# Optimization experiments

Measured on AMD Instinct MI355X. Metric: run time of the kernel, lower is better.

Reference implementation:

```python
import jax, jax.numpy as jnp
import numpy as np

EPS = 1e-6

def _phi(x):
    # elu(x) + 1 feature map
    return jax.nn.elu(x) + 1.0

def setup_inputs() -> dict:
    key = jax.random.key(0)
    kq, kk, kv = jax.random.split(key, 3)
    N, L, S, H, D, M = 8, 4096, 4096, 8, 64, 64
    queries = jax.random.normal(kq, (N, L, H, D), dtype=jnp.float32)
    keys = jax.random.normal(kk, (N, S, H, D), dtype=jnp.float32)
    values = jax.random.normal(kv, (N, S, H, M), dtype=jnp.float32)
    key_mask = jnp.ones((N, S), dtype=jnp.float32)  # key_lengths.float_matrix
    return {"queries": queries, "keys": keys, "values": values, "key_mask": key_mask}

def reference(queries, keys, values, key_mask):
    Q = _phi(queries)                                   # [N,L,H,D]
    K = _phi(keys) * key_mask[:, :, None, None]         # [N,S,H,D]
    KV = jnp.einsum('nshd,nshm->nhmd', K, values)       # [N,H,M,D]
    Z = 1.0 / (jnp.einsum('nlhd,nhd->nlh', Q, K.sum(axis=1)) + EPS)  # [N,L,H]
    V = jnp.einsum('nlhd,nhmd,nlh->nlhm', Q, KV, Z)     # [N,L,H,M]
    return V
```

## Files before the change

### kernel.cpp

```cpp
#include <hip/hip_runtime.h>


#define SLEN 4096
#define LLEN 4096
#define NB   8
#define HH   8
#define DD   64
#define MM   64
#define HD   512

__device__ __forceinline__ float phi(float x) {
    return x > 0.0f ? x + 1.0f : __expf(x);
}

__device__ __forceinline__ void fma4(float4& a, float s, float4 b) {
    a.x = fmaf(s, b.x, a.x);
    a.y = fmaf(s, b.y, a.y);
    a.z = fmaf(s, b.z, a.z);
    a.w = fmaf(s, b.w, a.w);
}

__global__ __launch_bounds__(256)
void la_phase1(const float* __restrict__ Kg, const float* __restrict__ Vg,
               const float* __restrict__ maskg,
               float* __restrict__ KVt, float* __restrict__ Ksum) {
    __shared__ float Ks[64 * 64];
    __shared__ float Vs[64 * 64];
    __shared__ float Red[64 * 68];
    __shared__ float KsB[16 * 64];

    const int tid  = threadIdx.x;
    const int nh   = blockIdx.y;
    const int n    = nh >> 3;
    const int h    = nh & 7;
    const int sbase = blockIdx.x * 512;

    const size_t base = (size_t)n * SLEN * HD + (size_t)h * DD;
    const float* mrow = maskg + (size_t)n * SLEN;

    const int col4 = (tid & 15) * 4;
    const int r0   = tid >> 4;

    const int lane = tid & 63;
    const int grp  = tid >> 6;
    const int d0   = (lane & 7) * 8;
    const int m0   = (lane >> 3) * 8;

    float4 acc[8][2];
    #pragma unroll
    for (int i = 0; i < 8; ++i) {
        acc[i][0] = make_float4(0.f, 0.f, 0.f, 0.f);
        acc[i][1] = make_float4(0.f, 0.f, 0.f, 0.f);
    }
    float4 ksp = make_float4(0.f, 0.f, 0.f, 0.f);

    for (int t = 0; t < 8; ++t) {
        const int srow0 = sbase + t * 64;
        #pragma unroll
        for (int rr = 0; rr < 4; ++rr) {
            const int row = r0 + rr * 16;
            const int s   = srow0 + row;
            const size_t goff = base + (size_t)s * HD + col4;
            float4 kf = *(const float4*)(Kg + goff);
            const float mmv = mrow[s];
            kf.x = phi(kf.x) * mmv;
            kf.y = phi(kf.y) * mmv;
            kf.z = phi(kf.z) * mmv;
            kf.w = phi(kf.w) * mmv;
            *(float4*)&Ks[row * 64 + col4] = kf;
            ksp.x += kf.x; ksp.y += kf.y; ksp.z += kf.z; ksp.w += kf.w;
            *(float4*)&Vs[row * 64 + col4] = *(const float4*)(Vg + goff);
        }
        __syncthreads();
        #pragma unroll 4
        for (int s = grp; s < 64; s += 4) {
            float4 ka = *(const float4*)&Ks[s * 64 + d0];
            float4 kb = *(const float4*)&Ks[s * 64 + d0 + 4];
            float4 va = *(const float4*)&Vs[s * 64 + m0];
            float4 vb = *(const float4*)&Vs[s * 64 + m0 + 4];
            const float kk[8] = {ka.x, ka.y, ka.z, ka.w, kb.x, kb.y, kb.z, kb.w};
            #pragma unroll
            for (int di = 0; di < 8; ++di) {
                fma4(acc[di][0], kk[di], va);
                fma4(acc[di][1], kk[di], vb);
            }
        }
        __syncthreads();
    }

    if (grp == 0) {
        #pragma unroll
        for (int di = 0; di < 8; ++di) {
            *(float4*)&Red[(d0 + di) * 68 + m0]     = acc[di][0];
            *(float4*)&Red[(d0 + di) * 68 + m0 + 4] = acc[di][1];
        }
    }
    __syncthreads();
    for (int g = 1; g < 4; ++g) {
        if (grp == g) {
            #pragma unroll
            for (int di = 0; di < 8; ++di) {
                float4* p0 = (float4*)&Red[(d0 + di) * 68 + m0];
                float4* p1 = (float4*)&Red[(d0 + di) * 68 + m0 + 4];
                float4 v0 = *p0, v1 = *p1;
                v0.x += acc[di][0].x; v0.y += acc[di][0].y; v0.z += acc[di][0].z; v0.w += acc[di][0].w;
                v1.x += acc[di][1].x; v1.y += acc[di][1].y; v1.z += acc[di][1].z; v1.w += acc[di][1].w;
                *p0 = v0; *p1 = v1;
            }
        }
        __syncthreads();
    }

    *(float4*)&KsB[r0 * 64 + col4] = ksp;
    __syncthreads();
    if (tid < 64) {
        float ssum = 0.f;
        #pragma unroll
        for (int r = 0; r < 16; ++r) ssum += KsB[r * 64 + tid];
        atomicAdd(&Ksum[nh * 64 + tid], ssum);
    }

    for (int k2 = 0; k2 < 16; ++k2) {
        const int idx = k2 * 256 + tid;
        atomicAdd(&KVt[(size_t)nh * 4096 + idx], Red[(idx >> 6) * 68 + (idx & 63)]);
    }
}

__global__ __launch_bounds__(128)
void la_phase2(const float* __restrict__ Qg, const float* __restrict__ KVt,
               const float* __restrict__ Ksum, float* __restrict__ Og) {
    __shared__ float Qs[128 * 68];
    __shared__ float KVs[64 * 64];
    __shared__ float KSs[64];

    const int tid = threadIdx.x;
    const int nh  = blockIdx.y;
    const int n   = nh >> 3;
    const int h   = nh & 7;
    const int lbase = blockIdx.x * 128;

    const int col4 = (tid & 15) * 4;
    const int r0   = tid >> 4;
    #pragma unroll
    for (int rr = 0; rr < 16; ++rr) {
        const int row = r0 + rr * 8;
        const int l   = lbase + row;
        float4 q = *(const float4*)&Qg[((size_t)(n * LLEN + l) * HH + h) * DD + col4];
        q.x = phi(q.x); q.y = phi(q.y); q.z = phi(q.z); q.w = phi(q.w);
        *(float4*)&Qs[row * 68 + col4] = q;
    }
    #pragma unroll
    for (int k2 = 0; k2 < 8; ++k2) {
        const int f = k2 * 128 + tid;
        *(float4*)&KVs[f * 4] = *(const float4*)&KVt[(size_t)nh * 4096 + f * 4];
    }
    if (tid < 16) *(float4*)&KSs[tid * 4] = *(const float4*)&Ksum[nh * 64 + tid * 4];
    __syncthreads();

    const int wv   = tid >> 6;
    const int lane = tid & 63;
    const int tx   = lane & 7;
    const int ty   = lane >> 3;
    const int rowbase = wv * 64 + ty;
    const int m0 = tx * 8;

    float4 acc[8][2];
    float  den[8];
    #pragma unroll
    for (int i = 0; i < 8; ++i) {
        acc[i][0] = make_float4(0.f, 0.f, 0.f, 0.f);
        acc[i][1] = make_float4(0.f, 0.f, 0.f, 0.f);
        den[i] = 0.f;
    }

    for (int d4 = 0; d4 < 16; ++d4) {
        float4 q4[8];
        #pragma unroll
        for (int i = 0; i < 8; ++i)
            q4[i] = *(const float4*)&Qs[(rowbase + 8 * i) * 68 + d4 * 4];
        const float4 ks = *(const float4*)&KSs[d4 * 4];
        #pragma unroll
        for (int i = 0; i < 8; ++i) {
            den[i] = fmaf(q4[i].x, ks.x, den[i]);
            den[i] = fmaf(q4[i].y, ks.y, den[i]);
            den[i] = fmaf(q4[i].z, ks.z, den[i]);
            den[i] = fmaf(q4[i].w, ks.w, den[i]);
        }
        #pragma unroll
        for (int dk = 0; dk < 4; ++dk) {
            const int d = d4 * 4 + dk;
            const float4 kv0 = *(const float4*)&KVs[d * 64 + m0];
            const float4 kv1 = *(const float4*)&KVs[d * 64 + m0 + 4];
            #pragma unroll
            for (int i = 0; i < 8; ++i) {
                const float qs = ((const float*)&q4[i])[dk];
                fma4(acc[i][0], qs, kv0);
                fma4(acc[i][1], qs, kv1);
            }
        }
    }

    #pragma unroll
    for (int i = 0; i < 8; ++i) {
        const int l = lbase + rowbase + 8 * i;
        const float z = 1.0f / (den[i] + 1e-6f);
        float4 o0 = acc[i][0], o1 = acc[i][1];
        o0.x *= z; o0.y *= z; o0.z *= z; o0.w *= z;
        o1.x *= z; o1.y *= z; o1.z *= z; o1.w *= z;
        const size_t off = ((size_t)(n * LLEN + l) * HH + h) * MM + m0;
        *(float4*)&Og[off]     = o0;
        *(float4*)&Og[off + 4] = o1;
    }
}

extern "C" void kernel_launch(void* const* d_in, const int* in_sizes, int n_in,
                              void* d_out, int out_size, void* d_ws, size_t ws_size,
                              hipStream_t stream) {
    const float* Q    = (const float*)d_in[0];
    const float* K    = (const float*)d_in[1];
    const float* V    = (const float*)d_in[2];
    const float* mask = (const float*)d_in[3];
    float* out  = (float*)d_out;
    float* KVt  = (float*)d_ws;
    float* Ksum = KVt + (size_t)NB * HH * DD * MM;

    hipMemsetAsync(d_ws, 0, ((size_t)NB * HH * DD * MM + (size_t)NB * HH * DD) * sizeof(float), stream);

    dim3 g1(SLEN / 512, NB * HH);
    la_phase1<<<g1, 256, 0, stream>>>(K, V, mask, KVt, Ksum);

    dim3 g2(LLEN / 128, NB * HH);
    la_phase2<<<g2, 128, 0, stream>>>(Q, KVt, Ksum, out);
}
```

Measured before the change: 262.7 us.

## Restructure linear attention into per-wave pipelined phase1, split reduce, register-Q phase2

Phase 1 now gives each wave its own LDS slab and register-prefetches the next K/V chunk, which removes block-wide barriers from the main loop. Partial KV and Ksum sums go to a workspace and a separate reduce kernel combines them, replacing global atomics and the memset. Phase 2 keeps each thread's Q row in registers and computes 16 outputs per thread, dropping the Q LDS staging. The cost is an extra kernel launch and extra workspace traffic, and phase 2 does less reuse per KV LDS load.

```diff
diff --git a/kernel.cpp b/kernel.cpp
--- a/kernel.cpp
+++ b/kernel.cpp
@@ -3,17 +3,16 @@
 
 #define SLEN 4096
 #define LLEN 4096
-#define NB   8
-#define HH   8
-#define DD   64
-#define MM   64
+#define NHTOT 64
 #define HD   512
+#define NSPLIT 8
+#define EPSF 1e-6f
 
 __device__ __forceinline__ float phi(float x) {
     return x > 0.0f ? x + 1.0f : __expf(x);
 }
 
-__device__ __forceinline__ void fma4(float4& a, float s, float4 b) {
+__device__ __forceinline__ void fma4(float4& a, float s, const float4& b) {
     a.x = fmaf(s, b.x, a.x);
     a.y = fmaf(s, b.y, a.y);
     a.z = fmaf(s, b.z, a.z);
@@ -23,194 +22,270 @@
 __global__ __launch_bounds__(256)
 void la_phase1(const float* __restrict__ Kg, const float* __restrict__ Vg,
                const float* __restrict__ maskg,
+               float* __restrict__ KVp, float* __restrict__ Ksump) {
+    __shared__ float lds[8448];
+
+    const int tid  = threadIdx.x;
+    const int w    = tid >> 6;
+    const int lane = tid & 63;
+    const int nh   = blockIdx.y;
+    const int n    = nh >> 3;
+    const int h    = nh & 7;
+    const int sp   = blockIdx.x;
+
+    const int r  = lane >> 4;
+    const int c4 = lane & 15;
+    const int d0 = (lane & 7) * 8;
+    const int m0 = (lane >> 3) * 8;
+
+    float* kb = lds + w * 2112;
+    float* vb = kb + 1088;
+
+    const size_t base = (size_t)n * SLEN * HD + (size_t)h * 64;
+    const float* mrow = maskg + (size_t)n * SLEN;
+    const int swave = sp * 512 + w * 128;
+
+    float4 acc[8][2];
+    #pragma unroll
+    for (int i = 0; i < 8; ++i) {
+        acc[i][0] = make_float4(0.f, 0.f, 0.f, 0.f);
+        acc[i][1] = make_float4(0.f, 0.f, 0.f, 0.f);
+    }
+    float4 ksp = make_float4(0.f, 0.f, 0.f, 0.f);
+
+    float4 kr[4], vr[4];
+    float  mr[4];
+    #pragma unroll
+    for (int j = 0; j < 4; ++j) {
+        const int s = swave + r + 4 * j;
+        const size_t g = base + (size_t)s * HD + c4 * 4;
+        kr[j] = *(const float4*)(Kg + g);
+        vr[j] = *(const float4*)(Vg + g);
+        mr[j] = mrow[s];
+    }
+
+    #pragma unroll 1
+    for (int t = 0; t < 8; ++t) {
+        float4 kn[4], vn[4];
+        float  mn[4];
+        if (t < 7) {
+            const int s0 = swave + (t + 1) * 16;
+            #pragma unroll
+            for (int j = 0; j < 4; ++j) {
+                const int s = s0 + r + 4 * j;
+                const size_t g = base + (size_t)s * HD + c4 * 4;
+                kn[j] = *(const float4*)(Kg + g);
+                vn[j] = *(const float4*)(Vg + g);
+                mn[j] = mrow[s];
+            }
+        }
+        #pragma unroll
+        for (int j = 0; j < 4; ++j) {
+            float4 kf = kr[j];
+            const float mm = mr[j];
+            kf.x = phi(kf.x) * mm;
+            kf.y = phi(kf.y) * mm;
+            kf.z = phi(kf.z) * mm;
+            kf.w = phi(kf.w) * mm;
+            ksp.x += kf.x; ksp.y += kf.y; ksp.z += kf.z; ksp.w += kf.w;
+            const int row = r + 4 * j;
+            *(float4*)&kb[row * 68 + c4 * 4] = kf;
+            *(float4*)&vb[row * 64 + c4 * 4] = vr[j];
+        }
+        #pragma unroll
+        for (int s = 0; s < 16; ++s) {
+            const float4 ka  = *(const float4*)&kb[s * 68 + d0];
+            const float4 kc  = *(const float4*)&kb[s * 68 + d0 + 4];
+            const float4 va  = *(const float4*)&vb[s * 64 + m0];
+            const float4 vc  = *(const float4*)&vb[s * 64 + m0 + 4];
+            const float kk[8] = {ka.x, ka.y, ka.z, ka.w, kc.x, kc.y, kc.z, kc.w};
+            #pragma unroll
+            for (int di = 0; di < 8; ++di) {
+                fma4(acc[di][0], kk[di], va);
+                fma4(acc[di][1], kk[di], vc);
+            }
+        }
+        if (t < 7) {
+            #pragma unroll
+            for (int j = 0; j < 4; ++j) { kr[j] = kn[j]; vr[j] = vn[j]; mr[j] = mn[j]; }
+        }
+    }
+
+    __syncthreads();
+
+    ksp.x += __shfl_xor(ksp.x, 16); ksp.y += __shfl_xor(ksp.y, 16);
+    ksp.z += __shfl_xor(ksp.z, 16); ksp.w += __shfl_xor(ksp.w, 16);
+    ksp.x += __shfl_xor(ksp.x, 32); ksp.y += __shfl_xor(ksp.y, 32);
+    ksp.z += __shfl_xor(ksp.z, 32); ksp.w += __shfl_xor(ksp.w, 32);
+    if (lane < 16) *(float4*)&lds[8192 + w * 64 + lane * 4] = ksp;
+
+    float* Red0 = lds;
+    float* Red1 = lds + 4096;
+    if (w == 2) {
+        #pragma unroll
+        for (int di = 0; di < 8; ++di) {
+            *(float4*)&Red0[(d0 + di) * 64 + m0]     = acc[di][0];
+            *(float4*)&Red0[(d0 + di) * 64 + m0 + 4] = acc[di][1];
+        }
+    }
+    if (w == 3) {
+        #pragma unroll
+        for (int di = 0; di < 8; ++di) {
+            *(float4*)&Red1[(d0 + di) * 64 + m0]     = acc[di][0];
+            *(float4*)&Red1[(d0 + di) * 64 + m0 + 4] = acc[di][1];
+        }
+    }
+    __syncthreads();
+    if (w == 0) {
+        #pragma unroll
+        for (int di = 0; di < 8; ++di) {
+            const float4 a = *(const float4*)&Red0[(d0 + di) * 64 + m0];
+            const float4 b = *(const float4*)&Red0[(d0 + di) * 64 + m0 + 4];
+            acc[di][0].x += a.x; acc[di][0].y += a.y; acc[di][0].z += a.z; acc[di][0].w += a.w;
+            acc[di][1].x += b.x; acc[di][1].y += b.y; acc[di][1].z += b.z; acc[di][1].w += b.w;
+        }
+    }
+    if (w == 1) {
+        #pragma unroll
+        for (int di = 0; di < 8; ++di) {
+            const float4 a = *(const float4*)&Red1[(d0 + di) * 64 + m0];
+            const float4 b = *(const float4*)&Red1[(d0 + di) * 64 + m0 + 4];
+            acc[di][0].x += a.x; acc[di][0].y += a.y; acc[di][0].z += a.z; acc[di][0].w += a.w;
+            acc[di][1].x += b.x; acc[di][1].y += b.y; acc[di][1].z += b.z; acc[di][1].w += b.w;
+        }
+    }
+    if (tid < 16) {
+        float4 s = make_float4(0.f, 0.f, 0.f, 0.f);
+        #pragma unroll
+        for (int ww = 0; ww < 4; ++ww) {
+            const float4 v = *(const float4*)&lds[8192 + ww * 64 + tid * 4];
+            s.x += v.x; s.y += v.y; s.z += v.z; s.w += v.w;
+        }
+        *(float4*)&Ksump[((size_t)sp * NHTOT + nh) * 64 + tid * 4] = s;
+    }
+    __syncthreads();
+    if (w == 1) {
+        #pragma unroll
+        for (int di = 0; di < 8; ++di) {
+            *(float4*)&Red0[(d0 + di) * 64 + m0]     = acc[di][0];
+            *(float4*)&Red0[(d0 + di) * 64 + m0 + 4] = acc[di][1];
+        }
+    }
+    __syncthreads();
+    if (w == 0) {
+        float* outp = KVp + ((size_t)sp * NHTOT + nh) * 4096;
+        #pragma unroll
+        for (int di = 0; di < 8; ++di) {
+            const float4 a = *(const float4*)&Red0[(d0 + di) * 64 + m0];
+            const float4 b = *(const float4*)&Red0[(d0 + di) * 64 + m0 + 4];
+            float4 o0 = acc[di][0], o1 = acc[di][1];
+            o0.x += a.x; o0.y += a.y; o0.z += a.z; o0.w += a.w;
+            o1.x += b.x; o1.y += b.y; o1.z += b.z; o1.w += b.w;
+            *(float4*)&outp[(d0 + di) * 64 + m0]     = o0;
+            *(float4*)&outp[(d0 + di) * 64 + m0 + 4] = o1;
+        }
+    }
+}
+
+__global__ __launch_bounds__(256)
+void la_reduce(const float* __restrict__ KVp, const float* __restrict__ Ksump,
                float* __restrict__ KVt, float* __restrict__ Ksum) {
-    __shared__ float Ks[64 * 64];
-    __shared__ float Vs[64 * 64];
-    __shared__ float Red[64 * 68];
-    __shared__ float KsB[16 * 64];
+    const int nh  = blockIdx.x;
+    const int tid = threadIdx.x;
+    #pragma unroll
+    for (int j = 0; j < 4; ++j) {
+        const int f = (j * 256 + tid) * 4;
+        float4 a = make_float4(0.f, 0.f, 0.f, 0.f);
+        #pragma unroll
+        for (int s = 0; s < NSPLIT; ++s) {
+            const float4 v = *(const float4*)&KVp[((size_t)s * NHTOT + nh) * 4096 + f];
+            a.x += v.x; a.y += v.y; a.z += v.z; a.w += v.w;
+        }
+        *(float4*)&KVt[(size_t)nh * 4096 + f] = a;
+    }
+    if (tid < 16) {
+        float4 a = make_float4(0.f, 0.f, 0.f, 0.f);
+        #pragma unroll
+        for (int s = 0; s < NSPLIT; ++s) {
+            const float4 v = *(const float4*)&Ksump[((size_t)s * NHTOT + nh) * 64 + tid * 4];
+            a.x += v.x; a.y += v.y; a.z += v.z; a.w += v.w;
+        }
+        *(float4*)&Ksum[nh * 64 + tid * 4] = a;
+    }
+}
+
+__global__ __launch_bounds__(256)
+void la_phase2(const float* __restrict__ Qg, const float* __restrict__ KVt,
+               const float* __restrict__ Ksum, float* __restrict__ Og) {
+    __shared__ float KVs[4096];
+    __shared__ float KSs[64];
 
     const int tid  = threadIdx.x;
     const int nh   = blockIdx.y;
     const int n    = nh >> 3;
     const int h    = nh & 7;
-    const int sbase = blockIdx.x * 512;
-
-    const size_t base = (size_t)n * SLEN * HD + (size_t)h * DD;
-    const float* mrow = maskg + (size_t)n * SLEN;
-
-    const int col4 = (tid & 15) * 4;
-    const int r0   = tid >> 4;
-
+    const int w    = tid >> 6;
     const int lane = tid & 63;
-    const int grp  = tid >> 6;
-    const int d0   = (lane & 7) * 8;
-    const int m0   = (lane >> 3) * 8;
-
-    float4 acc[8][2];
-    #pragma unroll
-    for (int i = 0; i < 8; ++i) {
-        acc[i][0] = make_float4(0.f, 0.f, 0.f, 0.f);
-        acc[i][1] = make_float4(0.f, 0.f, 0.f, 0.f);
-    }
-    float4 ksp = make_float4(0.f, 0.f, 0.f, 0.f);
-
-    for (int t = 0; t < 8; ++t) {
-        const int srow0 = sbase + t * 64;
-        #pragma unroll
-        for (int rr = 0; rr < 4; ++rr) {
-            const int row = r0 + rr * 16;
-            const int s   = srow0 + row;
-            const size_t goff = base + (size_t)s * HD + col4;
-            float4 kf = *(const float4*)(Kg + goff);
-            const float mmv = mrow[s];
-            kf.x = phi(kf.x) * mmv;
-            kf.y = phi(kf.y) * mmv;
-            kf.z = phi(kf.z) * mmv;
-            kf.w = phi(kf.w) * mmv;
-            *(float4*)&Ks[row * 64 + col4] = kf;
-            ksp.x += kf.x; ksp.y += kf.y; ksp.z += kf.z; ksp.w += kf.w;
-            *(float4*)&Vs[row * 64 + col4] = *(const float4*)(Vg + goff);
-        }
-        __syncthreads();
-        #pragma unroll 4
-        for (int s = grp; s < 64; s += 4) {
-            float4 ka = *(const float4*)&Ks[s * 64 + d0];
-            float4 kb = *(const float4*)&Ks[s * 64 + d0 + 4];
-            float4 va = *(const float4*)&Vs[s * 64 + m0];
-            float4 vb = *(const float4*)&Vs[s * 64 + m0 + 4];
-            const float kk[8] = {ka.x, ka.y, ka.z, ka.w, kb.x, kb.y, kb.z, kb.w};
-            #pragma unroll
-            for (int di = 0; di < 8; ++di) {
-                fma4(acc[di][0], kk[di], va);
-                fma4(acc[di][1], kk[di], vb);
-            }
-        }
-        __syncthreads();
-    }
-
-    if (grp == 0) {
-        #pragma unroll
-        for (int di = 0; di < 8; ++di) {
-            *(float4*)&Red[(d0 + di) * 68 + m0]     = acc[di][0];
-            *(float4*)&Red[(d0 + di) * 68 + m0 + 4] = acc[di][1];
-        }
-    }
-    __syncthreads();
-    for (int g = 1; g < 4; ++g) {
-        if (grp == g) {
-            #pragma unroll
-            for (int di = 0; di < 8; ++di) {
-                float4* p0 = (float4*)&Red[(d0 + di) * 68 + m0];
-                float4* p1 = (float4*)&Red[(d0 + di) * 68 + m0 + 4];
-                float4 v0 = *p0, v1 = *p1;
-                v0.x += acc[di][0].x; v0.y += acc[di][0].y; v0.z += acc[di][0].z; v0.w += acc[di][0].w;
-                v1.x += acc[di][1].x; v1.y += acc[di][1].y; v1.z += acc[di][1].z; v1.w += acc[di][1].w;
-                *p0 = v0; *p1 = v1;
-            }
-        }
-        __syncthreads();
-    }
-
-    *(float4*)&KsB[r0 * 64 + col4] = ksp;
-    __syncthreads();
-    if (tid < 64) {
-        float ssum = 0.f;
-        #pragma unroll
-        for (int r = 0; r < 16; ++r) ssum += KsB[r * 64 + tid];
-        atomicAdd(&Ksum[nh * 64 + tid], ssum);
-    }
-
-    for (int k2 = 0; k2 < 16; ++k2) {
-        const int idx = k2 * 256 + tid;
-        atomicAdd(&KVt[(size_t)nh * 4096 + idx], Red[(idx >> 6) * 68 + (idx & 63)]);
-    }
-}
-
-__global__ __launch_bounds__(128)
-void la_phase2(const float* __restrict__ Qg, const float* __restrict__ KVt,
-               const float* __restrict__ Ksum, float* __restrict__ Og) {
-    __shared__ float Qs[128 * 68];
-    __shared__ float KVs[64 * 64];
-    __shared__ float KSs[64];
-
-    const int tid = threadIdx.x;
-    const int nh  = blockIdx.y;
-    const int n   = nh >> 3;
-    const int h   = nh & 7;
-    const int lbase = blockIdx.x * 128;
-
-    const int col4 = (tid & 15) * 4;
-    const int r0   = tid >> 4;
-    #pragma unroll
-    for (int rr = 0; rr < 16; ++rr) {
-        const int row = r0 + rr * 8;
-        const int l   = lbase + row;
-        float4 q = *(const float4*)&Qg[((size_t)(n * LLEN + l) * HH + h) * DD + col4];
-        q.x = phi(q.x); q.y = phi(q.y); q.z = phi(q.z); q.w = phi(q.w);
-        *(float4*)&Qs[row * 68 + col4] = q;
-    }
-    #pragma unroll
-    for (int k2 = 0; k2 < 8; ++k2) {
-        const int f = k2 * 128 + tid;
-        *(float4*)&KVs[f * 4] = *(const float4*)&KVt[(size_t)nh * 4096 + f * 4];
+    const int ty   = lane >> 2;
+    const int tx   = lane & 3;
+    const int row  = blockIdx.x * 64 + w * 16 + ty;
+    const int m0   = tx * 16;
+
+    #pragma unroll
+    for (int j = 0; j < 4; ++j) {
+        const int f = (j * 256 + tid) * 4;
+        *(float4*)&KVs[f] = *(const float4*)&KVt[(size_t)nh * 4096 + f];
     }
     if (tid < 16) *(float4*)&KSs[tid * 4] = *(const float4*)&Ksum[nh * 64 + tid * 4];
-    __syncthreads();
-
-    const int wv   = tid >> 6;
-    const int lane = tid & 63;
-    const int tx   = lane & 7;
-    const int ty   = lane >> 3;
-    const int rowbase = wv * 64 + ty;
-    const int m0 = tx * 8;
-
-    float4 acc[8][2];
-    float  den[8];
-    #pragma unroll
-    for (int i = 0; i < 8; ++i) {
-        acc[i][0] = make_float4(0.f, 0.f, 0.f, 0.f);
-        acc[i][1] = make_float4(0.f, 0.f, 0.f, 0.f);
-        den[i] = 0.f;
-    }
-
-    for (int d4 = 0; d4 < 16; ++d4) {
-        float4 q4[8];
-        #pragma unroll
-        for (int i = 0; i < 8; ++i)
-            q4[i] = *(const float4*)&Qs[(rowbase + 8 * i) * 68 + d4 * 4];
-        const float4 ks = *(const float4*)&KSs[d4 * 4];
-        #pragma unroll
-        for (int i = 0; i < 8; ++i) {
-            den[i] = fmaf(q4[i].x, ks.x, den[i]);
-            den[i] = fmaf(q4[i].y, ks.y, den[i]);
-            den[i] = fmaf(q4[i].z, ks.z, den[i]);
-            den[i] = fmaf(q4[i].w, ks.w, den[i]);
-        }
+
+    const size_t qoff = ((size_t)(n * LLEN + row) * 8 + h) * 64;
+    float4 q[16];
+    #pragma unroll
+    for (int j = 0; j < 16; ++j) q[j] = *(const float4*)&Qg[qoff + j * 4];
+    #pragma unroll
+    for (int j = 0; j < 16; ++j) {
+        q[j].x = phi(q[j].x); q[j].y = phi(q[j].y);
+        q[j].z = phi(q[j].z); q[j].w = phi(q[j].w);
+    }
+    __syncthreads();
+
+    float4 a0 = make_float4(0.f, 0.f, 0.f, 0.f);
+    float4 a1 = a0, a2 = a0, a3 = a0;
+    float den = 0.f;
+
+    #pragma unroll
+    for (int j = 0; j < 16; ++j) {
+        const float4 q4 = q[j];
+        const float4 ks = *(const float4*)&KSs[j * 4];
+        den = fmaf(q4.x, ks.x, den);
+        den = fmaf(q4.y, ks.y, den);
+        den = fmaf(q4.z, ks.z, den);
+        den = fmaf(q4.w, ks.w, den);
         #pragma unroll
         for (int dk = 0; dk < 4; ++dk) {
-            const int d = d4 * 4 + dk;
+            const int d = j * 4 + dk;
+            const float qs = (&q4.x)[dk];
             const float4 kv0 = *(const float4*)&KVs[d * 64 + m0];
             const float4 kv1 = *(const float4*)&KVs[d * 64 + m0 + 4];
-            #pragma unroll
-            for (int i = 0; i < 8; ++i) {
-                const float qs = ((const float*)&q4[i])[dk];
-                fma4(acc[i][0], qs, kv0);
-                fma4(acc[i][1], qs, kv1);
-            }
-        }
-    }
-
-    #pragma unroll
-    for (int i = 0; i < 8; ++i) {
-        const int l = lbase + rowbase + 8 * i;
-        const float z = 1.0f / (den[i] + 1e-6f);
-        float4 o0 = acc[i][0], o1 = acc[i][1];
-        o0.x *= z; o0.y *= z; o0.z *= z; o0.w *= z;
-        o1.x *= z; o1.y *= z; o1.z *= z; o1.w *= z;
-        const size_t off = ((size_t)(n * LLEN + l) * HH + h) * MM + m0;
-        *(float4*)&Og[off]     = o0;
-        *(float4*)&Og[off + 4] = o1;
-    }
+            const float4 kv2 = *(const float4*)&KVs[d * 64 + m0 + 8];
+            const float4 kv3 = *(const float4*)&KVs[d * 64 + m0 + 12];
+            fma4(a0, qs, kv0);
+            fma4(a1, qs, kv1);
+            fma4(a2, qs, kv2);
+            fma4(a3, qs, kv3);
+        }
+    }
+
+    const float z = 1.0f / (den + EPSF);
+    a0.x *= z; a0.y *= z; a0.z *= z; a0.w *= z;
+    a1.x *= z; a1.y *= z; a1.z *= z; a1.w *= z;
+    a2.x *= z; a2.y *= z; a2.z *= z; a2.w *= z;
+    a3.x *= z; a3.y *= z; a3.z *= z; a3.w *= z;
+    float* op = Og + ((size_t)(n * LLEN + row) * 8 + h) * 64 + m0;
+    *(float4*)&op[0]  = a0;
+    *(float4*)&op[4]  = a1;
+    *(float4*)&op[8]  = a2;
+    *(float4*)&op[12] = a3;
 }
 
 extern "C" void kernel_launch(void* const* d_in, const int* in_sizes, int n_in,
@@ -220,15 +295,18 @@
     const float* K    = (const float*)d_in[1];
     const float* V    = (const float*)d_in[2];
     const float* mask = (const float*)d_in[3];
-    float* out  = (float*)d_out;
-    float* KVt  = (float*)d_ws;
-    float* Ksum = KVt + (size_t)NB * HH * DD * MM;
-
-    hipMemsetAsync(d_ws, 0, ((size_t)NB * HH * DD * MM + (size_t)NB * HH * DD) * sizeof(float), stream);
-
-    dim3 g1(SLEN / 512, NB * HH);
-    la_phase1<<<g1, 256, 0, stream>>>(K, V, mask, KVt, Ksum);
-
-    dim3 g2(LLEN / 128, NB * HH);
-    la_phase2<<<g2, 128, 0, stream>>>(Q, KVt, Ksum, out);
-}
+    float* out = (float*)d_out;
+
+    float* KVp   = (float*)d_ws;
+    float* Ksump = KVp + (size_t)NSPLIT * NHTOT * 4096;
+    float* KVt   = Ksump + (size_t)NSPLIT * NHTOT * 64;
+    float* Ksum  = KVt + (size_t)NHTOT * 4096;
+
+    dim3 g1(NSPLIT, NHTOT);
+    la_phase1<<<g1, 256, 0, stream>>>(K, V, mask, KVp, Ksump);
+
+    la_reduce<<<NHTOT, 256, 0, stream>>>(KVp, Ksump, KVt, Ksum);
+
+    dim3 g2(LLEN / 64, NHTOT);
+    la_phase2<<<g2, 256, 0, stream>>>(Q, KVt, Ksum, out);
+}
```

Result: slower. 278.7 us (+6.1%).
